# Kernel optimization log

Measured on AMD Instinct MI355X. Metric: run time of the kernel, lower is better.

The kernel has to match this reference:

```python
import jax, jax.numpy as jnp
import numpy as np
from jax import lax

B, DIM, DIM_OUT, NH = 8, 512, 512, 8
HD = DIM_OUT // NH          # 64, also the depthwise-conv channel count
SQ, SKV = (1, 1), (2, 2)    # stride_q, stride_kv
PAD = 1                      # kernel 3 -> padding 3//2
SCALE = HD ** -0.5
EPS = 1e-6


def _dw_conv(x, w, stride):
    # x: [N, C, H, W], w: [C, 1, kh, kw]; depthwise conv (groups = C), no bias
    return lax.conv_general_dilated(
        x, w, window_strides=stride, padding=[(PAD, PAD), (PAD, PAD)],
        dimension_numbers=('NCHW', 'OIHW', 'NCHW'),
        feature_group_count=x.shape[1])


def _ln(x, w, b):
    m = jnp.mean(x, -1, keepdims=True)
    v = jnp.var(x, -1, keepdims=True)
    return (x - m) * lax.rsqrt(v + EPS) * w + b


def _pool(t, w, stride, ln_w, ln_b, H, W):
    # t: [B, NH, 1+H*W, HD] with cls token at index 0
    Bn = t.shape[0]
    cls = t[:, :, :1, :]
    body = t[:, :, 1:, :].reshape(Bn * NH, H, W, HD).transpose(0, 3, 1, 2)
    body = _dw_conv(body, w, stride)
    ph, pw = body.shape[2], body.shape[3]
    body = body.reshape(Bn, NH, HD, ph * pw).transpose(0, 1, 3, 2)
    out = jnp.concatenate([cls, body], axis=2)
    return _ln(out, ln_w, ln_b), (ph, pw)


def _rel_bias(r_q4, q_shape, k_shape, rel_pos_h, rel_pos_w):
    # r_q4: [B, NH, q_h*q_w, HD] (cls token stripped)
    q_h, q_w = q_shape
    k_h, k_w = k_shape

    def dist(qs, ks):
        qr, kr = max(ks / qs, 1.0), max(qs / ks, 1.0)
        d = np.arange(qs)[:, None] * qr - np.arange(ks)[None, :] * kr + (ks - 1) * kr
        return d.astype(np.int64)

    Rh = rel_pos_h[dist(q_h, k_h)]  # [q_h, k_h, HD]
    Rw = rel_pos_w[dist(q_w, k_w)]  # [q_w, k_w, HD]
    r_q = r_q4.reshape(r_q4.shape[0], NH, q_h, q_w, HD)
    rel_h = jnp.einsum('byhwc,hkc->byhwk', r_q, Rh)  # [B,NH,q_h,q_w,k_h]
    rel_w = jnp.einsum('byhwc,wkc->byhwk', r_q, Rw)  # [B,NH,q_h,q_w,k_w]
    return rel_h[..., :, None] + rel_w[..., None, :]  # [B,NH,q_h,q_w,k_h,k_w]


def setup_inputs() -> dict:
    key = jax.random.key(0)
    ks = jax.random.split(key, 16)
    H = W = 56
    N = H * W + 1
    rel_dim = 2 * H - 1  # 111
    return {
        'x': jax.random.normal(ks[0], (B, N, DIM), jnp.float32),
        'qkv_w': jax.random.normal(ks[1], (3 * DIM_OUT, DIM), jnp.float32) * DIM ** -0.5,
        'qkv_b': jax.random.normal(ks[2], (3 * DIM_OUT,), jnp.float32) * 0.02,
        'proj_w': jax.random.normal(ks[3], (DIM_OUT, DIM_OUT), jnp.float32) * DIM_OUT ** -0.5,
        'proj_b': jax.random.normal(ks[4], (DIM_OUT,), jnp.float32) * 0.02,
        'pool_q_w': jax.random.normal(ks[5], (HD, 1, 3, 3), jnp.float32) / 3.0,
        'pool_k_w': jax.random.normal(ks[6], (HD, 1, 3, 3), jnp.float32) / 3.0,
        'pool_v_w': jax.random.normal(ks[7], (HD, 1, 3, 3), jnp.float32) / 3.0,
        'lnq_w': 1.0 + 0.1 * jax.random.normal(ks[8], (HD,), jnp.float32),
        'lnq_b': 0.02 * jax.random.normal(ks[9], (HD,), jnp.float32),
        'lnk_w': 1.0 + 0.1 * jax.random.normal(ks[10], (HD,), jnp.float32),
        'lnk_b': 0.02 * jax.random.normal(ks[11], (HD,), jnp.float32),
        'lnv_w': 1.0 + 0.1 * jax.random.normal(ks[12], (HD,), jnp.float32),
        'lnv_b': 0.02 * jax.random.normal(ks[13], (HD,), jnp.float32),
        'rel_pos_h': 0.02 * jax.random.normal(ks[14], (rel_dim, HD), jnp.float32),
        'rel_pos_w': 0.02 * jax.random.normal(ks[15], (rel_dim, HD), jnp.float32),
        'hw_h': 56,
        'hw_w': 56,
    }


def reference(x, qkv_w, qkv_b, proj_w, proj_b, pool_q_w, pool_k_w, pool_v_w,
              lnq_w, lnq_b, lnk_w, lnk_b, lnv_w, lnv_b, rel_pos_h, rel_pos_w,
              hw_h, hw_w):
    Bn, N, _ = x.shape
    qkv = (x @ qkv_w.T + qkv_b).reshape(Bn, N, 3, NH, HD).transpose(2, 0, 3, 1, 4)
    q, k, v = qkv[0], qkv[1], qkv[2]  # each [B, NH, N, HD]
    q, q_shape = _pool(q, pool_q_w, SQ, lnq_w, lnq_b, hw_h, hw_w)
    k, k_shape = _pool(k, pool_k_w, SKV, lnk_w, lnk_b, hw_h, hw_w)
    v, _ = _pool(v, pool_v_w, SKV, lnv_w, lnv_b, hw_h, hw_w)
    attn = (q * SCALE) @ k.swapaxes(-2, -1)  # [B, NH, Nq, Nk]
    q_h, q_w = q_shape
    k_h, k_w = k_shape
    bias = _rel_bias(q[:, :, 1:, :], q_shape, k_shape, rel_pos_h, rel_pos_w)
    blk = attn[:, :, 1:, 1:].reshape(Bn, NH, q_h, q_w, k_h, k_w) + bias
    attn = attn.at[:, :, 1:, 1:].set(blk.reshape(Bn, NH, q_h * q_w, k_h * k_w))
    attn = jax.nn.softmax(attn, axis=-1)
    out = attn @ v                                   # [B, NH, Nq, HD]
    out = out.at[:, :, 1:, :].add(q[:, :, 1:, :])    # residual on non-cls rows
    out = out.transpose(0, 2, 1, 3).reshape(Bn, -1, DIM_OUT)
    return out @ proj_w.T + proj_b
```

## Files before the change

kernel.cpp:

```cpp
#include <hip/hip_runtime.h>
#include <hip/hip_bf16.h>
#include <cstdint>
#include <cstddef>

#define BB 8
#define NHH 8
#define NQ 3137
#define NKV 785
#define HDIM 64
#define AUG 128
#define MROWS (BB*NQ)
#define SCALE 0.125f
#define VTP 832

typedef unsigned short ushort_t;
typedef __attribute__((ext_vector_type(8))) short s16x8;
typedef __attribute__((ext_vector_type(4))) float f32x4;
typedef __attribute__((ext_vector_type(16))) float f32x16;

__device__ __forceinline__ float bf2f(ushort_t u) {
  union { unsigned int i; float f; } v; v.i = ((unsigned int)u) << 16; return v.f;
}
__device__ __forceinline__ ushort_t f2bf(float f) {
  union { float f; unsigned int i; } v; v.f = f;
  unsigned int r = v.i + 0x7fffu + ((v.i >> 16) & 1u);
  return (ushort_t)(r >> 16);
}
__device__ __forceinline__ unsigned int cvt_pk_bf16(float lo, float hi) {
  unsigned int r;
  asm("v_cvt_pk_bf16_f32 %0, %1, %2" : "=v"(r) : "v"(lo), "v"(hi));
  return r;
}
__device__ __forceinline__ s16x8 lds_frag8(const ushort_t* base, int row, int slot) {
  const char* p = (const char*)base + row * 128 + (((slot ^ (row & 7)) & 7) << 4);
  return *(const s16x8*)p;
}
__device__ __forceinline__ s16x8 lds_frag16(const ushort_t* base, int row, int slot) {
  const char* p = (const char*)base + row * 256 + (((slot ^ (row & 15)) & 15) << 4);
  return *(const s16x8*)p;
}

template<int EPI, bool AF32, bool WF32>
__global__ __launch_bounds__(256) void mfma_gemm_bt(
    const void* __restrict__ Ap, const void* __restrict__ Wp,
    const float* __restrict__ bias, void* __restrict__ outp, int M) {
  __shared__ ushort_t As[128][40];
  __shared__ ushort_t Bs[128][40];
  const int tid = threadIdx.x;
  const int l = tid & 63, w = tid >> 6;
  const int wr = w >> 1, wc = w & 1;
  const int lrow = l & 15, lk = l >> 4;
  const int m0 = blockIdx.y * 128, n0 = blockIdx.x * 128;
  const int srow = tid >> 2, sch = tid & 3;
  const int mA0 = m0 + srow      < M ? m0 + srow      : M - 1;
  const int mA1 = m0 + 64 + srow < M ? m0 + 64 + srow : M - 1;
  const size_t ar0 = (size_t)mA0 * 512, ar1 = (size_t)mA1 * 512;
  const size_t br0 = (size_t)(n0 + srow) * 512, br1 = (size_t)(n0 + 64 + srow) * 512;
  const ushort_t* Ab = (const ushort_t*)Ap;
  const float*    Af = (const float*)Ap;
  const ushort_t* Wb = (const ushort_t*)Wp;
  const float*    Wf = (const float*)Wp;
  auto ld8 = [&](const ushort_t* pb, const float* pf, size_t ofs, bool f32) -> uint4 {
    if (!f32) return *(const uint4*)(pb + ofs);
    const float4 v0 = *(const float4*)(pf + ofs);
    const float4 v1 = *(const float4*)(pf + ofs + 4);
    uint4 r;
    r.x = cvt_pk_bf16(v0.x, v0.y); r.y = cvt_pk_bf16(v0.z, v0.w);
    r.z = cvt_pk_bf16(v1.x, v1.y); r.w = cvt_pk_bf16(v1.z, v1.w);
    return r;
  };
  f32x4 acc[4][4];
  #pragma unroll
  for (int i = 0; i < 4; ++i) {
    #pragma unroll
    for (int j = 0; j < 4; ++j) acc[i][j] = (f32x4){0.f, 0.f, 0.f, 0.f};
  }
  for (int k0 = 0; k0 < 512; k0 += 32) {
    const uint4 a0 = ld8(Ab, Af, ar0 + k0 + sch * 8, AF32);
    const uint4 a1 = ld8(Ab, Af, ar1 + k0 + sch * 8, AF32);
    const uint4 b0 = ld8(Wb, Wf, br0 + k0 + sch * 8, WF32);
    const uint4 b1 = ld8(Wb, Wf, br1 + k0 + sch * 8, WF32);
    __syncthreads();
    *(uint4*)(&As[srow][sch * 8])      = a0;
    *(uint4*)(&As[64 + srow][sch * 8]) = a1;
    *(uint4*)(&Bs[srow][sch * 8])      = b0;
    *(uint4*)(&Bs[64 + srow][sch * 8]) = b1;
    __syncthreads();
    s16x8 af[4], bfr[4];
    #pragma unroll
    for (int mi = 0; mi < 4; ++mi)
      af[mi] = *(const s16x8*)(&As[wr * 64 + mi * 16 + lrow][lk * 8]);
    #pragma unroll
    for (int ni = 0; ni < 4; ++ni)
      bfr[ni] = *(const s16x8*)(&Bs[wc * 64 + ni * 16 + lrow][lk * 8]);
    #pragma unroll
    for (int mi = 0; mi < 4; ++mi) {
      #pragma unroll
      for (int ni = 0; ni < 4; ++ni)
        acc[mi][ni] = __builtin_amdgcn_mfma_f32_16x16x32_bf16(
            af[mi], bfr[ni], acc[mi][ni], 0, 0, 0);
    }
  }
  #pragma unroll
  for (int mi = 0; mi < 4; ++mi) {
    #pragma unroll
    for (int r = 0; r < 4; ++r) {
      const int m = m0 + wr * 64 + mi * 16 + 4 * lk + r;
      if (m >= M) continue;
      #pragma unroll
      for (int ni = 0; ni < 4; ++ni) {
        const int n = n0 + wc * 64 + ni * 16 + lrow;
        const float v = acc[mi][ni][r] + bias[n];
        if (EPI == 0) {
          const int which = n >> 9, y = (n >> 6) & 7, c = n & 63;
          const int b_ = m / NQ, tok = m - b_ * NQ;
          ((ushort_t*)outp)[((((size_t)which * BB + b_) * NHH + y) * NQ + tok) * HDIM + c] = f2bf(v);
        } else {
          ((float*)outp)[(size_t)m * 512 + n] = v;
        }
      }
    }
  }
}

template<int MODE>
__global__ __launch_bounds__(256) void pool_ln_kernel(
    const ushort_t* __restrict__ in, ushort_t* __restrict__ out0,
    ushort_t* __restrict__ out1,
    const float* __restrict__ cw, const float* __restrict__ lnw,
    const float* __restrict__ lnb, int stride, int OW, int R) {
  const int tid = threadIdx.x;
  const int c = tid & 63;
  const int rid = blockIdx.x * 4 + (tid >> 6);
  const int by = rid / R;
  const int n = rid - by * R;
  const ushort_t* ibase = in + (size_t)by * NQ * HDIM;
  float val;
  if (n == 0) {
    val = bf2f(ibase[c]);
  } else {
    const int p = n - 1;
    const int ho = p / OW, wo = p - ho * OW;
    float s = 0.f;
    #pragma unroll
    for (int dh = 0; dh < 3; ++dh) {
      const int hh = ho * stride + dh - 1;
      if (hh < 0 || hh >= 56) continue;
      #pragma unroll
      for (int dw = 0; dw < 3; ++dw) {
        const int ww = wo * stride + dw - 1;
        if (ww < 0 || ww >= 56) continue;
        s += cw[c * 9 + dh * 3 + dw] * bf2f(ibase[(size_t)(1 + hh * 56 + ww) * HDIM + c]);
      }
    }
    val = s;
  }
  float sum = val, sq = val * val;
  #pragma unroll
  for (int off = 32; off > 0; off >>= 1) {
    sum += __shfl_xor(sum, off);
    sq  += __shfl_xor(sq,  off);
  }
  const float mean = sum * (1.f / 64.f);
  const float var  = sq * (1.f / 64.f) - mean * mean;
  const float rs = rsqrtf(var + 1e-6f);
  const float lno = (val - mean) * rs * lnw[c] + lnb[c];
  if (MODE == 0) {
    out0[(size_t)rid * HDIM + c] = f2bf(lno);
  } else if (MODE == 1) {
    out0[(size_t)rid * HDIM + c] = f2bf(lno);
    out1[(size_t)rid * AUG + c] = f2bf(lno * SCALE);
    out1[(size_t)rid * AUG + 64 + c] = 0;
  } else {
    out0[(size_t)rid * AUG + c] = f2bf(lno);
    ushort_t aug = 0;
    if (n >= 1) {
      const int p = n - 1;
      const int kh = p / 28, kw = p - 28 * kh;
      if (c < 28) { if (c == kh) aug = 0x3F80; }
      else if (c < 56) { if (c - 28 == kw) aug = 0x3F80; }
    }
    out0[(size_t)rid * AUG + 64 + c] = aug;
  }
}

__global__ __launch_bounds__(256) void transpose_v_kernel(
    const ushort_t* __restrict__ vin, ushort_t* __restrict__ vtout) {
  __shared__ ushort_t T[64][65];
  const int tid = threadIdx.x;
  const int by = blockIdx.y;
  const int n0 = blockIdx.x * 64;
  #pragma unroll
  for (int half = 0; half < 2; ++half) {
    const int idx = tid + half * 256;
    const int r = idx >> 3, s = idx & 7;
    const int n = n0 + r;
    uint4 d = make_uint4(0u, 0u, 0u, 0u);
    if (n < NKV) d = *(const uint4*)(vin + ((size_t)by * NKV + n) * HDIM + s * 8);
    const ushort_t* dp = (const ushort_t*)&d;
    #pragma unroll
    for (int e = 0; e < 8; ++e) T[r][s * 8 + e] = dp[e];
  }
  __syncthreads();
  #pragma unroll
  for (int half = 0; half < 2; ++half) {
    const int idx = tid + half * 256;
    const int c = idx >> 3, g = idx & 7;
    ushort_t pk[8];
    #pragma unroll
    for (int e = 0; e < 8; ++e) pk[e] = T[g * 8 + e][c];
    *(uint4*)(vtout + ((size_t)by * 64 + c) * VTP + n0 + g * 8) = *(const uint4*)pk;
  }
}

__global__ __launch_bounds__(256) void relbias_mfma_kernel(
    const ushort_t* __restrict__ qb, const float* __restrict__ rph,
    const float* __restrict__ rpw, ushort_t* __restrict__ qaug) {
  const int tid = threadIdx.x;
  const int l = tid & 63, w = tid >> 6;
  const int lrow = l & 15, lk = l >> 4;
  const int hw = blockIdx.y;
  const int mode = blockIdx.z;
  const int r0 = blockIdx.x * 256 + w * 64;
  const float* tab = mode ? rpw : rph;
  s16x8 bfr[2][2];
  #pragma unroll
  for (int ni = 0; ni < 2; ++ni) {
    const int kh = ni * 16 + lrow;
    int trow = hw - 2 * kh + 54;
    if (trow < 0) trow = 0;
    const float* tr = tab + (size_t)trow * 64 + lk * 8;
    #pragma unroll
    for (int k0 = 0; k0 < 2; ++k0) {
      const float4 t0 = *(const float4*)(tr + k0 * 32);
      const float4 t1 = *(const float4*)(tr + k0 * 32 + 4);
      s16x8 bb;
      bb[0] = (short)f2bf(t0.x); bb[1] = (short)f2bf(t0.y);
      bb[2] = (short)f2bf(t0.z); bb[3] = (short)f2bf(t0.w);
      bb[4] = (short)f2bf(t1.x); bb[5] = (short)f2bf(t1.y);
      bb[6] = (short)f2bf(t1.z); bb[7] = (short)f2bf(t1.w);
      bfr[ni][k0] = bb;
    }
  }
  s16x8 af[4][2];
  #pragma unroll
  for (int mi = 0; mi < 4; ++mi) {
    const int rA = r0 + mi * 16 + lrow;
    const int by = rA / 56, oth = rA - 56 * by;
    const int tok = mode ? (1 + oth * 56 + hw) : (1 + hw * 56 + oth);
    const ushort_t* qp = qb + ((size_t)by * NQ + tok) * HDIM + lk * 8;
    af[mi][0] = *(const s16x8*)(qp);
    af[mi][1] = *(const s16x8*)(qp + 32);
  }
  f32x4 acc[4][2];
  #pragma unroll
  for (int mi = 0; mi < 4; ++mi) {
    #pragma unroll
    for (int ni = 0; ni < 2; ++ni) acc[mi][ni] = (f32x4){0.f, 0.f, 0.f, 0.f};
  }
  #pragma unroll
  for (int k0 = 0; k0 < 2; ++k0) {
    #pragma unroll
    for (int mi = 0; mi < 4; ++mi) {
      #pragma unroll
      for (int ni = 0; ni < 2; ++ni)
        acc[mi][ni] = __builtin_amdgcn_mfma_f32_16x16x32_bf16(
            af[mi][k0], bfr[ni][k0], acc[mi][ni], 0, 0, 0);
    }
  }
  const int augofs = 64 + mode * 28;
  #pragma unroll
  for (int mi = 0; mi < 4; ++mi) {
    #pragma unroll
    for (int r = 0; r < 4; ++r) {
      const int row = r0 + mi * 16 + 4 * lk + r;
      const int by = row / 56, oth = row - 56 * by;
      const int tok = 1 + (mode ? (oth * 56 + hw) : (hw * 56 + oth));
      ushort_t* orow = qaug + ((size_t)by * NQ + tok) * AUG + augofs;
      #pragma unroll
      for (int ni = 0; ni < 2; ++ni) {
        const int kh = ni * 16 + lrow;
        if (kh < 28) orow[kh] = f2bf(acc[mi][ni][r]);
      }
    }
  }
}

__global__ __launch_bounds__(256) void attn_mfma32_kernel(
    const ushort_t* __restrict__ qaug, const ushort_t* __restrict__ kaug,
    const ushort_t* __restrict__ qb, const ushort_t* __restrict__ vt,
    ushort_t* __restrict__ outp) {
  __shared__ ushort_t Kl[64 * AUG];
  __shared__ ushort_t Vl[64 * 64];
  const int tid = threadIdx.x;
  const int l = tid & 63, w = tid >> 6;
  const int h = l >> 5, q5 = l & 31;
  const int by = blockIdx.y;
  const int qt0 = blockIdx.x * 128;
  const int qloc = w * 32 + q5;
  const int qglob = qt0 + qloc;
  const int qcl = qglob < NQ ? qglob : NQ - 1;
  const ushort_t* qrow = qaug + ((size_t)by * NQ + qcl) * AUG;
  s16x8 qf[8];
  #pragma unroll
  for (int cb = 0; cb < 8; ++cb)
    qf[cb] = *(const s16x8*)(qrow + cb * 16 + h * 8);
  f32x16 ot0, ot1;
  #pragma unroll
  for (int i = 0; i < 16; ++i) { ot0[i] = 0.f; ot1[i] = 0.f; }
  float mr = -1e30f, lr = 0.f;
  const int krow = tid >> 2, ks4 = (tid & 3) * 4;
  const int vrow = tid >> 3, vslot = tid & 7;
  int jK = krow; if (jK > NKV - 1) jK = NKV - 1;
  #pragma unroll 1
  for (int it = 0; it < 13; ++it) {
    const int j0 = it * 64;
    jK = j0 + krow; if (jK > NKV - 1) jK = NKV - 1;
    const ushort_t* ksrc = kaug + ((size_t)by * NKV + jK) * AUG + ks4 * 8;
    const uint4 kd0 = *(const uint4*)(ksrc);
    const uint4 kd1 = *(const uint4*)(ksrc + 8);
    const uint4 kd2 = *(const uint4*)(ksrc + 16);
    const uint4 kd3 = *(const uint4*)(ksrc + 24);
    const uint4 vd0 = *(const uint4*)(vt + ((size_t)by * 64 + vrow) * VTP + j0 + vslot * 8);
    const uint4 vd1 = *(const uint4*)(vt + ((size_t)by * 64 + vrow + 32) * VTP + j0 + vslot * 8);
    __syncthreads();
    {
      char* kbase = (char*)Kl + krow * 256;
      const int rm = krow & 15;
      *(uint4*)(kbase + (((ks4 + 0) ^ rm) << 4)) = kd0;
      *(uint4*)(kbase + (((ks4 + 1) ^ rm) << 4)) = kd1;
      *(uint4*)(kbase + (((ks4 + 2) ^ rm) << 4)) = kd2;
      *(uint4*)(kbase + (((ks4 + 3) ^ rm) << 4)) = kd3;
      *(uint4*)((char*)Vl + vrow * 128 + (((vslot ^ (vrow & 7)) & 7) << 4)) = vd0;
      *(uint4*)((char*)Vl + (vrow + 32) * 128 + (((vslot ^ ((vrow + 32) & 7)) & 7) << 4)) = vd1;
    }
    __syncthreads();
    f32x16 st0, st1;
    #pragma unroll
    for (int i = 0; i < 16; ++i) { st0[i] = 0.f; st1[i] = 0.f; }
    #pragma unroll
    for (int cb = 0; cb < 8; ++cb) {
      st0 = __builtin_amdgcn_mfma_f32_32x32x16_bf16(
          lds_frag16(Kl, q5, cb * 2 + h), qf[cb], st0, 0, 0, 0);
      st1 = __builtin_amdgcn_mfma_f32_32x32x16_bf16(
          lds_frag16(Kl, 32 + q5, cb * 2 + h), qf[cb], st1, 0, 0, 0);
    }
    float pa[16], pb[16];
    #pragma unroll
    for (int r = 0; r < 16; ++r) { pa[r] = st0[r]; pb[r] = st1[r]; }
    if (it == 12) {
      #pragma unroll
      for (int r = 0; r < 16; ++r) {
        const int klocal = (r & 3) + 8 * (r >> 2) + 4 * h;
        if (768 + klocal >= NKV) pa[r] = -1e30f;
        pb[r] = -1e30f;
      }
    }
    float mloc = pa[0];
    #pragma unroll
    for (int r = 1; r < 16; ++r) mloc = fmaxf(mloc, pa[r]);
    #pragma unroll
    for (int r = 0; r < 16; ++r) mloc = fmaxf(mloc, pb[r]);
    mloc = fmaxf(mloc, __shfl_xor(mloc, 32));
    const float mn = fmaxf(mr, mloc);
    const float sc = __expf(mr - mn);
    mr = mn;
    float ps = 0.f;
    #pragma unroll
    for (int r = 0; r < 16; ++r) { pa[r] = __expf(pa[r] - mn); ps += pa[r]; }
    #pragma unroll
    for (int r = 0; r < 16; ++r) { pb[r] = __expf(pb[r] - mn); ps += pb[r]; }
    ps += __shfl_xor(ps, 32);
    lr = lr * sc + ps;
    #pragma unroll
    for (int i = 0; i < 16; ++i) { ot0[i] *= sc; ot1[i] *= sc; }
    auto pvstep = [&](const float (&pv)[16], int kt) {
      #pragma unroll
      for (int kbk = 0; kbk < 2; ++kbk) {
        const unsigned int pk01 = cvt_pk_bf16(pv[kbk * 8 + 0], pv[kbk * 8 + 1]);
        const unsigned int pk23 = cvt_pk_bf16(pv[kbk * 8 + 2], pv[kbk * 8 + 3]);
        const unsigned int pk45 = cvt_pk_bf16(pv[kbk * 8 + 4], pv[kbk * 8 + 5]);
        const unsigned int pk67 = cvt_pk_bf16(pv[kbk * 8 + 6], pv[kbk * 8 + 7]);
        const unsigned int sA = (unsigned int)__shfl_xor((int)pk01, 32);
        const unsigned int sB = (unsigned int)__shfl_xor((int)pk45, 32);
        const unsigned int sC = (unsigned int)__shfl_xor((int)pk23, 32);
        const unsigned int sD = (unsigned int)__shfl_xor((int)pk67, 32);
        int4 fw;
        fw.x = (int)(h ? sB : pk01);
        fw.y = (int)(h ? sD : pk23);
        fw.z = (int)(h ? pk45 : sA);
        fw.w = (int)(h ? pk67 : sC);
        s16x8 pf;
        __builtin_memcpy(&pf, &fw, 16);
        const int slot = kt * 4 + kbk * 2 + h;
        ot0 = __builtin_amdgcn_mfma_f32_32x32x16_bf16(
            lds_frag8(Vl, q5, slot), pf, ot0, 0, 0, 0);
        ot1 = __builtin_amdgcn_mfma_f32_32x32x16_bf16(
            lds_frag8(Vl, 32 + q5, slot), pf, ot1, 0, 0, 0);
      }
    };
    pvstep(pa, 0);
    pvstep(pb, 1);
  }
  const float inv = 1.f / lr;
  if (qglob < NQ) {
    const int b_ = by >> 3, y_ = by & 7;
    ushort_t* obase = outp + ((size_t)b_ * NQ + qglob) * 512 + (size_t)y_ * 64;
    const ushort_t* rbase = qb + ((size_t)by * NQ + qglob) * HDIM;
    #pragma unroll
    for (int ch = 0; ch < 2; ++ch) {
      #pragma unroll
      for (int rg = 0; rg < 4; ++rg) {
        const int c0 = ch * 32 + 8 * rg + 4 * h;
        float vv[4];
        #pragma unroll
        for (int e = 0; e < 4; ++e)
          vv[e] = (ch ? ot1[rg * 4 + e] : ot0[rg * 4 + e]) * inv;
        if (qglob > 0) {
          #pragma unroll
          for (int e = 0; e < 4; ++e) vv[e] += bf2f(rbase[c0 + e]);
        }
        ushort_t pk[4] = { f2bf(vv[0]), f2bf(vv[1]), f2bf(vv[2]), f2bf(vv[3]) };
        *(uint2*)(obase + c0) = *(const uint2*)pk;
      }
    }
  }
}

extern "C" void kernel_launch(void* const* d_in, const int* in_sizes, int n_in,
                              void* d_out, int out_size, void* d_ws, size_t ws_size,
                              hipStream_t stream) {
  const float* x        = (const float*)d_in[0];
  const float* qkv_w    = (const float*)d_in[1];
  const float* qkv_b    = (const float*)d_in[2];
  const float* proj_w   = (const float*)d_in[3];
  const float* proj_b   = (const float*)d_in[4];
  const float* pool_q_w = (const float*)d_in[5];
  const float* pool_k_w = (const float*)d_in[6];
  const float* pool_v_w = (const float*)d_in[7];
  const float* lnq_w    = (const float*)d_in[8];
  const float* lnq_b    = (const float*)d_in[9];
  const float* lnk_w    = (const float*)d_in[10];
  const float* lnk_b    = (const float*)d_in[11];
  const float* lnv_w    = (const float*)d_in[12];
  const float* lnv_b    = (const float*)d_in[13];
  const float* rel_pos_h = (const float*)d_in[14];
  const float* rel_pos_w = (const float*)d_in[15];

  constexpr size_t E1 = (size_t)BB * NHH * NQ * HDIM;
  char* ws = (char*)d_ws;
  size_t off = 0;
  ushort_t* qkv_raw = (ushort_t*)(ws + off); off += 3 * E1 * 2;
  ushort_t* q_bf    = (ushort_t*)(ws + off); off += E1 * 2;
  ushort_t* qaug    = (ushort_t*)(ws + off); off += (size_t)BB * NHH * NQ * AUG * 2;
  ushort_t* kaug    = (ushort_t*)(ws + off); off += (size_t)BB * NHH * NKV * AUG * 2;
  ushort_t* v_bf    = (ushort_t*)(ws + off); off += (size_t)BB * NHH * NKV * HDIM * 2;
  ushort_t* v_t     = (ushort_t*)(ws + off); off += (size_t)64 * 64 * VTP * 2;
  ushort_t* attn_bf = qkv_raw;

  mfma_gemm_bt<0, true, true><<<dim3(12, 197), 256, 0, stream>>>(
      x, qkv_w, qkv_b, (void*)qkv_raw, MROWS);

  pool_ln_kernel<1><<<(64 * NQ) / 4,  256, 0, stream>>>(qkv_raw,          q_bf, qaug, pool_q_w, lnq_w, lnq_b, 1, 56, NQ);
  pool_ln_kernel<2><<<(64 * NKV) / 4, 256, 0, stream>>>(qkv_raw + E1,     kaug, nullptr, pool_k_w, lnk_w, lnk_b, 2, 28, NKV);
  pool_ln_kernel<0><<<(64 * NKV) / 4, 256, 0, stream>>>(qkv_raw + 2 * E1, v_bf, nullptr, pool_v_w, lnv_w, lnv_b, 2, 28, NKV);

  transpose_v_kernel<<<dim3(13, 64), 256, 0, stream>>>(v_bf, v_t);

  relbias_mfma_kernel<<<dim3(14, 56, 2), 256, 0, stream>>>(q_bf, rel_pos_h, rel_pos_w, qaug);

  attn_mfma32_kernel<<<dim3(25, 64), 256, 0, stream>>>(qaug, kaug, q_bf, v_t, attn_bf);

  mfma_gemm_bt<1, false, true><<<dim3(4, 197), 256, 0, stream>>>(
      attn_bf, proj_w, proj_b, d_out, MROWS);
}
```

Baseline: 472.6 us.

## Double-buffer K/V tiles in attention and skip rescale when max is stable

```diff
diff --git a/kernel.cpp b/kernel.cpp
--- a/kernel.cpp
+++ b/kernel.cpp
@@ -290,10 +290,11 @@
     const ushort_t* __restrict__ qaug, const ushort_t* __restrict__ kaug,
     const ushort_t* __restrict__ qb, const ushort_t* __restrict__ vt,
     ushort_t* __restrict__ outp) {
-  __shared__ ushort_t Kl[64 * AUG];
-  __shared__ ushort_t Vl[64 * 64];
+  __shared__ ushort_t Kl[2][64 * AUG];
+  __shared__ ushort_t Vl[2][64 * 64];
   const int tid = threadIdx.x;
-  const int l = tid & 63, w = tid >> 6;
+  const int l = tid & 63;
+  const int w = tid >> 6;
   const int h = l >> 5, q5 = l & 31;
   const int by = blockIdx.y;
   const int qt0 = blockIdx.x * 128;
@@ -311,40 +312,51 @@
   float mr = -1e30f, lr = 0.f;
   const int krow = tid >> 2, ks4 = (tid & 3) * 4;
   const int vrow = tid >> 3, vslot = tid & 7;
-  int jK = krow; if (jK > NKV - 1) jK = NKV - 1;
+  const ushort_t* kbase = kaug + (size_t)by * NKV * AUG + ks4 * 8;
+  const ushort_t* vbase0 = vt + ((size_t)by * 64 + vrow) * VTP + vslot * 8;
+  const ushort_t* vbase1 = vt + ((size_t)by * 64 + vrow + 32) * VTP + vslot * 8;
+  uint4 kreg[4], vreg[2];
+  auto load_tile = [&](int j0) {
+    int jK = j0 + krow; if (jK > NKV - 1) jK = NKV - 1;
+    const ushort_t* ksrc = kbase + (size_t)jK * AUG;
+    kreg[0] = *(const uint4*)(ksrc);
+    kreg[1] = *(const uint4*)(ksrc + 8);
+    kreg[2] = *(const uint4*)(ksrc + 16);
+    kreg[3] = *(const uint4*)(ksrc + 24);
+    vreg[0] = *(const uint4*)(vbase0 + j0);
+    vreg[1] = *(const uint4*)(vbase1 + j0);
+  };
+  auto store_tile = [&](int buf) {
+    char* kb_ = (char*)&Kl[buf][0] + krow * 256;
+    const int rm = krow & 15;
+    *(uint4*)(kb_ + (((ks4 + 0) ^ rm) << 4)) = kreg[0];
+    *(uint4*)(kb_ + (((ks4 + 1) ^ rm) << 4)) = kreg[1];
+    *(uint4*)(kb_ + (((ks4 + 2) ^ rm) << 4)) = kreg[2];
+    *(uint4*)(kb_ + (((ks4 + 3) ^ rm) << 4)) = kreg[3];
+    *(uint4*)((char*)&Vl[buf][0] + vrow * 128 + (((vslot ^ (vrow & 7)) & 7) << 4)) = vreg[0];
+    *(uint4*)((char*)&Vl[buf][0] + (vrow + 32) * 128 + (((vslot ^ ((vrow + 32) & 7)) & 7) << 4)) = vreg[1];
+  };
+  load_tile(0);
+  store_tile(0);
+  load_tile(64);
   #pragma unroll 1
   for (int it = 0; it < 13; ++it) {
-    const int j0 = it * 64;
-    jK = j0 + krow; if (jK > NKV - 1) jK = NKV - 1;
-    const ushort_t* ksrc = kaug + ((size_t)by * NKV + jK) * AUG + ks4 * 8;
-    const uint4 kd0 = *(const uint4*)(ksrc);
-    const uint4 kd1 = *(const uint4*)(ksrc + 8);
-    const uint4 kd2 = *(const uint4*)(ksrc + 16);
-    const uint4 kd3 = *(const uint4*)(ksrc + 24);
-    const uint4 vd0 = *(const uint4*)(vt + ((size_t)by * 64 + vrow) * VTP + j0 + vslot * 8);
-    const uint4 vd1 = *(const uint4*)(vt + ((size_t)by * 64 + vrow + 32) * VTP + j0 + vslot * 8);
-    __syncthreads();
-    {
-      char* kbase = (char*)Kl + krow * 256;
-      const int rm = krow & 15;
-      *(uint4*)(kbase + (((ks4 + 0) ^ rm) << 4)) = kd0;
-      *(uint4*)(kbase + (((ks4 + 1) ^ rm) << 4)) = kd1;
-      *(uint4*)(kbase + (((ks4 + 2) ^ rm) << 4)) = kd2;
-      *(uint4*)(kbase + (((ks4 + 3) ^ rm) << 4)) = kd3;
-      *(uint4*)((char*)Vl + vrow * 128 + (((vslot ^ (vrow & 7)) & 7) << 4)) = vd0;
-      *(uint4*)((char*)Vl + (vrow + 32) * 128 + (((vslot ^ ((vrow + 32) & 7)) & 7) << 4)) = vd1;
-    }
+    const int cur = it & 1;
+    const ushort_t* Kc = &Kl[cur][0];
+    const ushort_t* Vc = &Vl[cur][0];
     __syncthreads();
     f32x16 st0, st1;
     #pragma unroll
     for (int i = 0; i < 16; ++i) { st0[i] = 0.f; st1[i] = 0.f; }
+    __builtin_amdgcn_s_setprio(1);
     #pragma unroll
     for (int cb = 0; cb < 8; ++cb) {
       st0 = __builtin_amdgcn_mfma_f32_32x32x16_bf16(
-          lds_frag16(Kl, q5, cb * 2 + h), qf[cb], st0, 0, 0, 0);
+          lds_frag16(Kc, q5, cb * 2 + h), qf[cb], st0, 0, 0, 0);
       st1 = __builtin_amdgcn_mfma_f32_32x32x16_bf16(
-          lds_frag16(Kl, 32 + q5, cb * 2 + h), qf[cb], st1, 0, 0, 0);
-    }
+          lds_frag16(Kc, 32 + q5, cb * 2 + h), qf[cb], st1, 0, 0, 0);
+    }
+    __builtin_amdgcn_s_setprio(0);
     float pa[16], pb[16];
     #pragma unroll
     for (int r = 0; r < 16; ++r) { pa[r] = st0[r]; pb[r] = st1[r]; }
@@ -362,18 +374,21 @@
     #pragma unroll
     for (int r = 0; r < 16; ++r) mloc = fmaxf(mloc, pb[r]);
     mloc = fmaxf(mloc, __shfl_xor(mloc, 32));
-    const float mn = fmaxf(mr, mloc);
-    const float sc = __expf(mr - mn);
-    mr = mn;
+    if (!__all(mloc <= mr + 8.f)) {
+      const float mn = fmaxf(mr, mloc);
+      const float sc = __expf(mr - mn);
+      mr = mn;
+      lr *= sc;
+      #pragma unroll
+      for (int i = 0; i < 16; ++i) { ot0[i] *= sc; ot1[i] *= sc; }
+    }
     float ps = 0.f;
     #pragma unroll
-    for (int r = 0; r < 16; ++r) { pa[r] = __expf(pa[r] - mn); ps += pa[r]; }
-    #pragma unroll
-    for (int r = 0; r < 16; ++r) { pb[r] = __expf(pb[r] - mn); ps += pb[r]; }
+    for (int r = 0; r < 16; ++r) { pa[r] = __expf(pa[r] - mr); ps += pa[r]; }
+    #pragma unroll
+    for (int r = 0; r < 16; ++r) { pb[r] = __expf(pb[r] - mr); ps += pb[r]; }
     ps += __shfl_xor(ps, 32);
-    lr = lr * sc + ps;
-    #pragma unroll
-    for (int i = 0; i < 16; ++i) { ot0[i] *= sc; ot1[i] *= sc; }
+    lr += ps;
     auto pvstep = [&](const float (&pv)[16], int kt) {
       #pragma unroll
       for (int kbk = 0; kbk < 2; ++kbk) {
@@ -393,14 +408,20 @@
         s16x8 pf;
         __builtin_memcpy(&pf, &fw, 16);
         const int slot = kt * 4 + kbk * 2 + h;
+        __builtin_amdgcn_s_setprio(1);
         ot0 = __builtin_amdgcn_mfma_f32_32x32x16_bf16(
-            lds_frag8(Vl, q5, slot), pf, ot0, 0, 0, 0);
+            lds_frag8(Vc, q5, slot), pf, ot0, 0, 0, 0);
         ot1 = __builtin_amdgcn_mfma_f32_32x32x16_bf16(
-            lds_frag8(Vl, 32 + q5, slot), pf, ot1, 0, 0, 0);
+            lds_frag8(Vc, 32 + q5, slot), pf, ot1, 0, 0, 0);
+        __builtin_amdgcn_s_setprio(0);
       }
     };
     pvstep(pa, 0);
     pvstep(pb, 1);
+    if (it < 12) {
+      store_tile(cur ^ 1);
+      if (it < 11) load_tile((it + 2) * 64);
+    }
   }
   const float inv = 1.f / lr;
   if (qglob < NQ) {
```

New measurement: 546.7 us. 1.16x slower.

## Pre-cast GEMM operands to bf16 and stage tiles via direct global-to-LDS loads

Applied to the files above, without the earlier changes.

```diff
diff --git a/kernel.cpp b/kernel.cpp
--- a/kernel.cpp
+++ b/kernel.cpp
@@ -40,65 +40,70 @@
   return *(const s16x8*)p;
 }
 
-template<int EPI, bool AF32, bool WF32>
-__global__ __launch_bounds__(256) void mfma_gemm_bt(
-    const void* __restrict__ Ap, const void* __restrict__ Wp,
+__global__ __launch_bounds__(256) void cast_bf16_kernel(
+    const float* __restrict__ in, ushort_t* __restrict__ outp, int n4) {
+  const int i = blockIdx.x * 256 + threadIdx.x;
+  if (i >= n4) return;
+  const float4 v = ((const float4*)in)[i];
+  uint2 o;
+  o.x = cvt_pk_bf16(v.x, v.y);
+  o.y = cvt_pk_bf16(v.z, v.w);
+  *(uint2*)(outp + (size_t)i * 4) = o;
+}
+
+template<int EPI>
+__global__ __launch_bounds__(256) void mfma_gemm_glds(
+    const ushort_t* __restrict__ A, const ushort_t* __restrict__ W,
     const float* __restrict__ bias, void* __restrict__ outp, int M) {
-  __shared__ ushort_t As[128][40];
-  __shared__ ushort_t Bs[128][40];
+  __shared__ ushort_t As[128 * 64];
+  __shared__ ushort_t Bs[128 * 64];
   const int tid = threadIdx.x;
   const int l = tid & 63, w = tid >> 6;
   const int wr = w >> 1, wc = w & 1;
   const int lrow = l & 15, lk = l >> 4;
   const int m0 = blockIdx.y * 128, n0 = blockIdx.x * 128;
-  const int srow = tid >> 2, sch = tid & 3;
-  const int mA0 = m0 + srow      < M ? m0 + srow      : M - 1;
-  const int mA1 = m0 + 64 + srow < M ? m0 + 64 + srow : M - 1;
-  const size_t ar0 = (size_t)mA0 * 512, ar1 = (size_t)mA1 * 512;
-  const size_t br0 = (size_t)(n0 + srow) * 512, br1 = (size_t)(n0 + 64 + srow) * 512;
-  const ushort_t* Ab = (const ushort_t*)Ap;
-  const float*    Af = (const float*)Ap;
-  const ushort_t* Wb = (const ushort_t*)Wp;
-  const float*    Wf = (const float*)Wp;
-  auto ld8 = [&](const ushort_t* pb, const float* pf, size_t ofs, bool f32) -> uint4 {
-    if (!f32) return *(const uint4*)(pb + ofs);
-    const float4 v0 = *(const float4*)(pf + ofs);
-    const float4 v1 = *(const float4*)(pf + ofs + 4);
-    uint4 r;
-    r.x = cvt_pk_bf16(v0.x, v0.y); r.y = cvt_pk_bf16(v0.z, v0.w);
-    r.z = cvt_pk_bf16(v1.x, v1.y); r.w = cvt_pk_bf16(v1.z, v1.w);
-    return r;
-  };
+  const int lr8 = l >> 3;
+  const int swzch = ((l & 7) ^ lr8) * 8;
   f32x4 acc[4][4];
   #pragma unroll
   for (int i = 0; i < 4; ++i) {
     #pragma unroll
     for (int j = 0; j < 4; ++j) acc[i][j] = (f32x4){0.f, 0.f, 0.f, 0.f};
   }
-  for (int k0 = 0; k0 < 512; k0 += 32) {
-    const uint4 a0 = ld8(Ab, Af, ar0 + k0 + sch * 8, AF32);
-    const uint4 a1 = ld8(Ab, Af, ar1 + k0 + sch * 8, AF32);
-    const uint4 b0 = ld8(Wb, Wf, br0 + k0 + sch * 8, WF32);
-    const uint4 b1 = ld8(Wb, Wf, br1 + k0 + sch * 8, WF32);
+  for (int k0 = 0; k0 < 512; k0 += 64) {
     __syncthreads();
-    *(uint4*)(&As[srow][sch * 8])      = a0;
-    *(uint4*)(&As[64 + srow][sch * 8]) = a1;
-    *(uint4*)(&Bs[srow][sch * 8])      = b0;
-    *(uint4*)(&Bs[64 + srow][sch * 8]) = b1;
+    #pragma unroll
+    for (int j = 0; j < 4; ++j) {
+      const int rb = (w * 4 + j) * 8 + lr8;
+      int mA = m0 + rb; if (mA > M - 1) mA = M - 1;
+      const ushort_t* sa = A + (size_t)mA * 512 + k0 + swzch;
+      const ushort_t* sb = W + (size_t)(n0 + rb) * 512 + k0 + swzch;
+      __builtin_amdgcn_global_load_lds((void*)sa, (void*)(As + (w * 4 + j) * 512), 16, 0, 0);
+      __builtin_amdgcn_global_load_lds((void*)sb, (void*)(Bs + (w * 4 + j) * 512), 16, 0, 0);
+    }
     __syncthreads();
-    s16x8 af[4], bfr[4];
-    #pragma unroll
-    for (int mi = 0; mi < 4; ++mi)
-      af[mi] = *(const s16x8*)(&As[wr * 64 + mi * 16 + lrow][lk * 8]);
-    #pragma unroll
-    for (int ni = 0; ni < 4; ++ni)
-      bfr[ni] = *(const s16x8*)(&Bs[wc * 64 + ni * 16 + lrow][lk * 8]);
-    #pragma unroll
-    for (int mi = 0; mi < 4; ++mi) {
-      #pragma unroll
-      for (int ni = 0; ni < 4; ++ni)
-        acc[mi][ni] = __builtin_amdgcn_mfma_f32_16x16x32_bf16(
-            af[mi], bfr[ni], acc[mi][ni], 0, 0, 0);
+    #pragma unroll
+    for (int sub = 0; sub < 2; ++sub) {
+      s16x8 af[4], bfr[4];
+      #pragma unroll
+      for (int mi = 0; mi < 4; ++mi) {
+        const int r = wr * 64 + mi * 16 + lrow;
+        const int slot = (sub * 4 + lk) ^ (r & 7);
+        af[mi] = *(const s16x8*)(As + r * 64 + slot * 8);
+      }
+      #pragma unroll
+      for (int ni = 0; ni < 4; ++ni) {
+        const int r = wc * 64 + ni * 16 + lrow;
+        const int slot = (sub * 4 + lk) ^ (r & 7);
+        bfr[ni] = *(const s16x8*)(Bs + r * 64 + slot * 8);
+      }
+      #pragma unroll
+      for (int mi = 0; mi < 4; ++mi) {
+        #pragma unroll
+        for (int ni = 0; ni < 4; ++ni)
+          acc[mi][ni] = __builtin_amdgcn_mfma_f32_16x16x32_bf16(
+              af[mi], bfr[ni], acc[mi][ni], 0, 0, 0);
+      }
     }
   }
   #pragma unroll
@@ -311,11 +316,10 @@
   float mr = -1e30f, lr = 0.f;
   const int krow = tid >> 2, ks4 = (tid & 3) * 4;
   const int vrow = tid >> 3, vslot = tid & 7;
-  int jK = krow; if (jK > NKV - 1) jK = NKV - 1;
   #pragma unroll 1
   for (int it = 0; it < 13; ++it) {
     const int j0 = it * 64;
-    jK = j0 + krow; if (jK > NKV - 1) jK = NKV - 1;
+    int jK = j0 + krow; if (jK > NKV - 1) jK = NKV - 1;
     const ushort_t* ksrc = kaug + ((size_t)by * NKV + jK) * AUG + ks4 * 8;
     const uint4 kd0 = *(const uint4*)(ksrc);
     const uint4 kd1 = *(const uint4*)(ksrc + 8);
@@ -450,16 +454,23 @@
   constexpr size_t E1 = (size_t)BB * NHH * NQ * HDIM;
   char* ws = (char*)d_ws;
   size_t off = 0;
-  ushort_t* qkv_raw = (ushort_t*)(ws + off); off += 3 * E1 * 2;
-  ushort_t* q_bf    = (ushort_t*)(ws + off); off += E1 * 2;
-  ushort_t* qaug    = (ushort_t*)(ws + off); off += (size_t)BB * NHH * NQ * AUG * 2;
-  ushort_t* kaug    = (ushort_t*)(ws + off); off += (size_t)BB * NHH * NKV * AUG * 2;
-  ushort_t* v_bf    = (ushort_t*)(ws + off); off += (size_t)BB * NHH * NKV * HDIM * 2;
-  ushort_t* v_t     = (ushort_t*)(ws + off); off += (size_t)64 * 64 * VTP * 2;
-  ushort_t* attn_bf = qkv_raw;
-
-  mfma_gemm_bt<0, true, true><<<dim3(12, 197), 256, 0, stream>>>(
-      x, qkv_w, qkv_b, (void*)qkv_raw, MROWS);
+  ushort_t* x_bf     = (ushort_t*)(ws + off); off += (size_t)MROWS * 512 * 2;
+  ushort_t* qkvw_bf  = (ushort_t*)(ws + off); off += (size_t)1536 * 512 * 2;
+  ushort_t* projw_bf = (ushort_t*)(ws + off); off += (size_t)512 * 512 * 2;
+  ushort_t* qkv_raw  = (ushort_t*)(ws + off); off += 3 * E1 * 2;
+  ushort_t* q_bf     = (ushort_t*)(ws + off); off += E1 * 2;
+  ushort_t* qaug     = (ushort_t*)(ws + off); off += (size_t)BB * NHH * NQ * AUG * 2;
+  ushort_t* kaug     = (ushort_t*)(ws + off); off += (size_t)BB * NHH * NKV * AUG * 2;
+  ushort_t* v_bf     = (ushort_t*)(ws + off); off += (size_t)BB * NHH * NKV * HDIM * 2;
+  ushort_t* v_t      = (ushort_t*)(ws + off); off += (size_t)64 * 64 * VTP * 2;
+  ushort_t* attn_bf  = qkv_raw;
+
+  cast_bf16_kernel<<<(MROWS * 512 / 4 + 255) / 256, 256, 0, stream>>>(x, x_bf, MROWS * 512 / 4);
+  cast_bf16_kernel<<<768, 256, 0, stream>>>(qkv_w, qkvw_bf, 1536 * 512 / 4);
+  cast_bf16_kernel<<<256, 256, 0, stream>>>(proj_w, projw_bf, 512 * 512 / 4);
+
+  mfma_gemm_glds<0><<<dim3(12, 197), 256, 0, stream>>>(
+      x_bf, qkvw_bf, qkv_b, (void*)qkv_raw, MROWS);
 
   pool_ln_kernel<1><<<(64 * NQ) / 4,  256, 0, stream>>>(qkv_raw,          q_bf, qaug, pool_q_w, lnq_w, lnq_b, 1, 56, NQ);
   pool_ln_kernel<2><<<(64 * NKV) / 4, 256, 0, stream>>>(qkv_raw + E1,     kaug, nullptr, pool_k_w, lnk_w, lnk_b, 2, 28, NKV);
@@ -471,6 +482,6 @@
 
   attn_mfma32_kernel<<<dim3(25, 64), 256, 0, stream>>>(qaug, kaug, q_bf, v_t, attn_bf);
 
-  mfma_gemm_bt<1, false, true><<<dim3(4, 197), 256, 0, stream>>>(
-      attn_bf, proj_w, proj_b, d_out, MROWS);
-}
+  mfma_gemm_glds<1><<<dim3(4, 197), 256, 0, stream>>>(
+      attn_bf, projw_bf, proj_b, d_out, MROWS);
+}
```

New measurement: 447.5 us. 5.3% less time.
